# Kernel optimization log

Measured on AMD Instinct MI355X. Metric: run time of the kernel, lower is better.

The kernel has to match this reference:

```python
import jax, jax.numpy as jnp
import numpy as np

B = 32768
D_IN = 512      # input_dim == dict_dim (forced by the STE add)
HID = 512       # hard-coded hidden width of linear1
D = 512         # dict_dim / embedding_dim
P = 8           # per_factor_dict_size: number of codebooks / MLP branches
K = 10          # num_factor: codebook size (rows per embedding table)
COMMIT = 0.25


def setup_inputs() -> dict:
    key = jax.random.key(0)
    ks = jax.random.split(key, 7)
    s1 = 1.0 / np.sqrt(D_IN)
    s2 = 1.0 / np.sqrt(HID)
    return {
        "inputs": jax.random.normal(ks[0], (B, D_IN), jnp.float32),
        "W1": jax.random.uniform(ks[1], (P, HID, D_IN), jnp.float32, -s1, s1),
        "b1": jax.random.uniform(ks[2], (P, HID), jnp.float32, -s1, s1),
        "W2": jax.random.uniform(ks[3], (P, D, HID), jnp.float32, -s2, s2),
        "b2": jax.random.uniform(ks[4], (P, D), jnp.float32, -s2, s2),
        # embedding init: uniform(-1/num_factor, 1/num_factor)
        "E": jax.random.uniform(ks[5], (P, K, D), jnp.float32, -1.0 / K, 1.0 / K),
        "label_gen": jax.random.randint(ks[6], (B,), 0, K, jnp.int64),
    }


def reference(inputs, W1, b1, W2, b2, E, label_gen):
    sg = jax.lax.stop_gradient
    # P parallel 2-layer MLPs: [P, B, D]
    h = jax.nn.relu(jnp.einsum("bd,phd->pbh", inputs, W1) + b1[:, None, :])
    z = jnp.einsum("pbh,peh->pbe", h, W2) + b2[:, None, :]
    # squared-distance expansion per codebook: [P, B, K]
    distances = (
        jnp.sum(z * z, axis=-1, keepdims=True)
        + jnp.sum(E * E, axis=-1)[:, None, :]
        - 2.0 * jnp.einsum("pbd,pkd->pbk", z, E)
    )
    ave_distances = jnp.mean(distances, axis=0)          # [B, K]
    idx = jnp.argmin(ave_distances, axis=1)              # [B]
    # one-hot @ E[p] then mean over p == mean codebook gathered at idx
    Emean = jnp.mean(E, axis=0)                          # [K, D]
    vq = Emean[idx]                                      # [B, D]
    vq_z = inputs + sg(vq - inputs)                      # straight-through
    # all_vq_z[j] = mean_p E[p, j]; losses vs every code row: [K, B]
    diff1 = Emean[:, None, :] - sg(inputs)[None, :, :]   # [K, B, D]
    diff2 = sg(Emean)[:, None, :] - inputs[None, :, :]
    all_vq_loss = jnp.sum(diff1 * diff1, axis=-1) + COMMIT * jnp.sum(diff2 * diff2, axis=-1)
    all_vq_z = inputs[None, :, :] + sg(Emean[:, None, :] - inputs[None, :, :])  # [K, B, D]
    changed_vq_z = Emean[label_gen]                      # [B, D]
    return (vq_z, distances, all_vq_z, all_vq_loss, changed_vq_z)
```

## Files before the change

kernel.cpp:

```cpp
#include <hip/hip_runtime.h>
#include <stdint.h>

typedef _Float16 f16;
typedef _Float16 f16x4 __attribute__((ext_vector_type(4)));
typedef _Float16 f16x8 __attribute__((ext_vector_type(8)));
typedef float f32x4 __attribute__((ext_vector_type(4)));

#define B_ROWS 32768
#define DIM 512
#define NP 8
#define NK 10

typedef __attribute__((address_space(3))) unsigned int lds_u32;
typedef __attribute__((address_space(1))) const unsigned int gbl_u32;

__device__ __forceinline__ void gload_lds16(const void* g, void* l) {
  __builtin_amdgcn_global_load_lds((gbl_u32*)(uintptr_t)g, (lds_u32*)(uintptr_t)l, 16, 0, 0);
}


__global__ void prep_split(const float4* __restrict__ X4, f16x4* __restrict__ Xh4,
                           f16x4* __restrict__ Xl4, const float4* __restrict__ W14,
                           f16x4* __restrict__ W1h4, f16x4* __restrict__ W1l4,
                           const float4* __restrict__ W24, f16x4* __restrict__ W2h4) {
  int bid = blockIdx.x, tid = threadIdx.x;
  if (bid < 1024) {
    for (int i = bid * 256 + tid; i < 4194304; i += 1024 * 256) {
      float4 v = X4[i];
      f16x4 h = {(f16)v.x, (f16)v.y, (f16)v.z, (f16)v.w};
      f16x4 l = {(f16)(v.x - (float)h[0]), (f16)(v.y - (float)h[1]),
                 (f16)(v.z - (float)h[2]), (f16)(v.w - (float)h[3])};
      Xh4[i] = h;
      Xl4[i] = l;
    }
  } else if (bid < 1152) {
    for (int i = (bid - 1024) * 256 + tid; i < 524288; i += 128 * 256) {
      float4 v = W14[i];
      f16x4 h = {(f16)v.x, (f16)v.y, (f16)v.z, (f16)v.w};
      f16x4 l = {(f16)(v.x - (float)h[0]), (f16)(v.y - (float)h[1]),
                 (f16)(v.z - (float)h[2]), (f16)(v.w - (float)h[3])};
      W1h4[i] = h;
      W1l4[i] = l;
    }
  } else {
    for (int i = (bid - 1152) * 256 + tid; i < 524288; i += 128 * 256) {
      float4 v = W24[i];
      f16x4 h = {(f16)v.x, (f16)v.y, (f16)v.z, (f16)v.w};
      W2h4[i] = h;
    }
  }
}


__global__ void enorm2(const float* __restrict__ E, float* __restrict__ Emean,
                       float* __restrict__ E2, float* __restrict__ E2m) {
  int bid = blockIdx.x;
  int lane = threadIdx.x;
  if (bid < 80) {
    const float* src = E + (size_t)bid * DIM;
    float s = 0.f;
    for (int i = lane; i < DIM; i += 64) {
      float v = src[i];
      s = fmaf(v, v, s);
    }
#pragma unroll
    for (int m = 1; m < 64; m <<= 1) s += __shfl_xor(s, m, 64);
    if (lane == 0) E2[bid] = s;
  } else {
    int k = bid - 80;
    float acc = 0.f;
    for (int i = lane; i < DIM; i += 64) {
      float s = 0.f;
#pragma unroll
      for (int p = 0; p < NP; ++p) s += E[p * NK * DIM + k * DIM + i];
      s *= 0.125f;
      Emean[k * DIM + i] = s;
      acc = fmaf(s, s, acc);
    }
#pragma unroll
    for (int m = 1; m < 64; m <<= 1) acc += __shfl_xor(acc, m, 64);
    if (lane == 0) E2m[k] = acc;
  }
}


__global__ __launch_bounds__(512) void etilde_kernel(const float* __restrict__ W2,
                                                     const float* __restrict__ b2,
                                                     const float* __restrict__ E,
                                                     f16* __restrict__ EimgH,
                                                     f16* __restrict__ EimgL,
                                                     float* __restrict__ c_) {
  const int p = blockIdx.x / NK, k = blockIdx.x % NK;
  const int h = threadIdx.x;
  __shared__ float Er[512];
  __shared__ float red[8];
  Er[h] = E[((size_t)p * NK + k) * DIM + h];
  __syncthreads();
  const float* Wp = W2 + (size_t)p * DIM * DIM;
  float s = 0.f;
#pragma unroll 8
  for (int d = 0; d < DIM; ++d) s = fmaf(Wp[(size_t)d * DIM + h], Er[d], s);
  int ei = p * 8320 + k * 520 + h;
  f16 hi = (f16)s;
  EimgH[ei] = hi;
  EimgL[ei] = (f16)(s - (float)hi);
  if (h < 8) {
    int pi = p * 8320 + k * 520 + 512 + h;
    EimgH[pi] = (f16)0.f;
    EimgL[pi] = (f16)0.f;
  }
  if (k == 0) {
    for (int j = h; j < 6 * 520; j += 512) {
      int pi = p * 8320 + 10 * 520 + j;
      EimgH[pi] = (f16)0.f;
      EimgL[pi] = (f16)0.f;
    }
  }
  float t = b2[p * DIM + h] * Er[h];
#pragma unroll
  for (int m = 1; m < 64; m <<= 1) t += __shfl_xor(t, m, 64);
  if ((h & 63) == 0) red[h >> 6] = t;
  __syncthreads();
  if (h == 0) {
    float cc = 0.f;
#pragma unroll
    for (int i = 0; i < 8; ++i) cc += red[i];
    c_[p * NK + k] = cc;
  }
}


template <int EPI, int NBN, int NPROD, int GRP>
__global__ __launch_bounds__(256) void gemmA(
    const f16* __restrict__ Ah_, const f16* __restrict__ Al_, int lda, int apitch,
    const f16* __restrict__ Bh_, const f16* __restrict__ Bl_, int bpitch,
    const float* __restrict__ bias_, int bias_pitch,
    f16* __restrict__ Oh, f16* __restrict__ Ol, int ldo,
    float* __restrict__ part2) {
  __shared__ f16 smem[32768];
  const int tid = threadIdx.x;
  const int lane = tid & 63;
  const int wave = tid >> 6;
  const int wr = wave >> 1, wc = wave & 1;
  const int p = blockIdx.z;

  const int q8 = gridDim.x >> 3;
  const int bid = blockIdx.x;
  const int swz = (bid & 7) * q8 + (bid >> 3);
  const int band = swz / (GRP * NBN);
  const int r_ = swz % (GRP * NBN);
  const int bm = band * GRP + (r_ % GRP);
  const int bn = r_ / GRP;
  const int m0 = bm * 128, n0 = bn * 128;

  const f16* Ahp = Ah_ + (size_t)p * apitch;
  const f16* Alp = Al_ + (size_t)p * apitch;
  const f16* Bhp = Bh_ + (size_t)p * bpitch;
  const f16* Blp = Bl_ + (size_t)p * bpitch;

  const int NT = (NPROD == 3) ? 24 : 8;

  f32x4 acc[4][4] = {};

  auto stage = [&](int buf, int t) {
    const f16* As;
    const f16* Bs;
    int k0;
    if (NPROD == 3) {
      int pr = t % 3;
      As = (pr == 2) ? Alp : Ahp;
      Bs = (pr == 1) ? Blp : Bhp;
      k0 = (t / 3) * 64;
    } else {
      As = Ahp;
      Bs = Bhp;
      k0 = t * 64;
    }
    f16* sA = smem + buf * 16384;
    f16* sB = sA + 8192;
#pragma unroll
    for (int j = 0; j < 4; ++j) {
      int r = j * 32 + (tid >> 3);
      int c = ((tid & 7) ^ (r & 7)) * 8;
      gload_lds16(As + (size_t)(m0 + r) * lda + k0 + c, sA + j * 2048 + tid * 8);
      gload_lds16(Bs + (size_t)(n0 + r) * 512 + k0 + c, sB + j * 2048 + tid * 8);
    }
  };

  stage(0, 0);
  __syncthreads();

  const int g = lane >> 4, rl = lane & 15;

  for (int s = 0; s < NT; ++s) {
    int nx = s + 1;
    if (nx < NT) stage(nx & 1, nx);
    const char* sA = (const char*)(smem + (s & 1) * 16384);
    const char* sB = sA + 16384;
    f16x8 af[4][2], bf[4][2];
#pragma unroll
    for (int i = 0; i < 4; ++i) {
      int ra = wr * 64 + i * 16 + rl;
      int rb = wc * 64 + i * 16 + rl;
#pragma unroll
      for (int kk = 0; kk < 2; ++kk) {
        int cb = kk * 64 + g * 16;
        af[i][kk] = *(const f16x8*)(sA + ra * 128 + (cb ^ ((ra & 7) << 4)));
        bf[i][kk] = *(const f16x8*)(sB + rb * 128 + (cb ^ ((rb & 7) << 4)));
      }
    }
#pragma unroll
    for (int i = 0; i < 4; ++i)
#pragma unroll
      for (int jn = 0; jn < 4; ++jn)
#pragma unroll
        for (int kk = 0; kk < 2; ++kk)
          acc[i][jn] = __builtin_amdgcn_mfma_f32_16x16x32_f16(af[i][kk], bf[jn][kk], acc[i][jn], 0, 0, 0);
    __syncthreads();
  }

  if (EPI == 0) {
#pragma unroll
    for (int jn = 0; jn < 4; ++jn) {
      int cg = n0 + wc * 64 + jn * 16 + rl;
      float bv = bias_[cg];
#pragma unroll
      for (int i = 0; i < 4; ++i) {
        int r0 = m0 + wr * 64 + i * 16 + g * 4;
#pragma unroll
        for (int r = 0; r < 4; ++r) {
          float z = acc[i][jn][r] + bv;
          z = fmaxf(z, 0.f);
          f16 h = (f16)z;
          size_t off = (size_t)(r0 + r) * ldo + cg;
          Oh[off] = h;
          Ol[off] = (f16)(z - (float)h);
        }
      }
    }
  } else {
    const float* bp = bias_ + (size_t)p * bias_pitch;
    float bvals[4];
#pragma unroll
    for (int jn = 0; jn < 4; ++jn) bvals[jn] = bp[n0 + wc * 64 + jn * 16 + rl];
    const int ch = bn * 2 + wc;
    float* pb = part2 + (size_t)(p * 8 + ch) * B_ROWS;
#pragma unroll
    for (int i = 0; i < 4; ++i) {
#pragma unroll
      for (int r = 0; r < 4; ++r) {
        float q = 0.f;
#pragma unroll
        for (int jn = 0; jn < 4; ++jn) {
          float z = acc[i][jn][r] + bvals[jn];
          q = fmaf(z, z, q);
        }
#pragma unroll
        for (int m = 1; m < 16; m <<= 1) q += __shfl_xor(q, m, 64);
        if (rl == 0) pb[m0 + wr * 64 + i * 16 + g * 4 + r] = q;
      }
    }
  }
}


__global__ __launch_bounds__(256) void g2d_union(
    const f16* __restrict__ Hh, const f16* __restrict__ Hl,
    const f16* __restrict__ W2h, const float* __restrict__ b2,
    const f16* __restrict__ EimgH, const f16* __restrict__ EimgL,
    const float* __restrict__ c_, float* __restrict__ part2,
    float* __restrict__ gout) {
  __shared__ char pool[66048];
  const int tid = threadIdx.x;
  const int p = blockIdx.y;

  if (blockIdx.x < 1024) {
    f16* smem = (f16*)pool;
    const int lane = tid & 63, wave = tid >> 6;
    const int wr = wave >> 1, wc = wave & 1;
    const int bid = blockIdx.x;
    const int swz = (bid & 7) * 128 + (bid >> 3);
    const int bm = swz >> 2, bn = swz & 3;
    const int m0 = bm * 128, n0 = bn * 128;
    const f16* Ahp = Hh + (size_t)p * 512;
    const f16* Bhp = W2h + (size_t)p * 262144;

    f32x4 acc[4][4] = {};

    auto stage = [&](int buf, int t) {
      int k0 = t * 64;
      f16* sA = smem + buf * 16384;
      f16* sB = sA + 8192;
#pragma unroll
      for (int j = 0; j < 4; ++j) {
        int r = j * 32 + (tid >> 3);
        int c = ((tid & 7) ^ (r & 7)) * 8;
        gload_lds16(Ahp + (size_t)(m0 + r) * 4096 + k0 + c, sA + j * 2048 + tid * 8);
        gload_lds16(Bhp + (size_t)(n0 + r) * 512 + k0 + c, sB + j * 2048 + tid * 8);
      }
    };

    stage(0, 0);
    __syncthreads();
    const int g = lane >> 4, rl = lane & 15;
    for (int s = 0; s < 8; ++s) {
      if (s + 1 < 8) stage((s + 1) & 1, s + 1);
      const char* sA = (const char*)(smem + (s & 1) * 16384);
      const char* sB = sA + 16384;
      f16x8 af[4][2], bf[4][2];
#pragma unroll
      for (int i = 0; i < 4; ++i) {
        int ra = wr * 64 + i * 16 + rl;
        int rb = wc * 64 + i * 16 + rl;
#pragma unroll
        for (int kk = 0; kk < 2; ++kk) {
          int cb = kk * 64 + g * 16;
          af[i][kk] = *(const f16x8*)(sA + ra * 128 + (cb ^ ((ra & 7) << 4)));
          bf[i][kk] = *(const f16x8*)(sB + rb * 128 + (cb ^ ((rb & 7) << 4)));
        }
      }
#pragma unroll
      for (int i = 0; i < 4; ++i)
#pragma unroll
        for (int jn = 0; jn < 4; ++jn)
#pragma unroll
          for (int kk = 0; kk < 2; ++kk)
            acc[i][jn] = __builtin_amdgcn_mfma_f32_16x16x32_f16(af[i][kk], bf[jn][kk], acc[i][jn], 0, 0, 0);
      __syncthreads();
    }

    const float* bp = b2 + (size_t)p * 512;
    float bvals[4];
#pragma unroll
    for (int jn = 0; jn < 4; ++jn) bvals[jn] = bp[n0 + wc * 64 + jn * 16 + rl];
    const int ch = bn * 2 + wc;
    float* pb = part2 + (size_t)(p * 8 + ch) * B_ROWS;
#pragma unroll
    for (int i = 0; i < 4; ++i) {
#pragma unroll
      for (int r = 0; r < 4; ++r) {
        float q = 0.f;
#pragma unroll
        for (int jn = 0; jn < 4; ++jn) {
          float z = acc[i][jn][r] + bvals[jn];
          q = fmaf(z, z, q);
        }
#pragma unroll
        for (int m = 1; m < 16; m <<= 1) q += __shfl_xor(q, m, 64);
        if (rl == 0) pb[m0 + wr * 64 + i * 16 + g * 4 + r] = q;
      }
    }
  } else {
    f16* sH = (f16*)pool;
    f16* sL = (f16*)(pool + 16384);
    f16* sEh = (f16*)(pool + 32768);
    f16* sEl = (f16*)(pool + 49408);
    const int lane = tid & 63, wave = tid >> 6;
    const int r0 = (blockIdx.x - 1024) * 64;
    {
      const uint32_t* ih = (const uint32_t*)(EimgH + (size_t)p * 16 * 520);
      const uint32_t* il = (const uint32_t*)(EimgL + (size_t)p * 16 * 520);
      uint32_t* oh = (uint32_t*)sEh;
      uint32_t* ol = (uint32_t*)sEl;
      for (int i = tid; i < 16 * 520 / 2; i += 256) {
        oh[i] = ih[i];
        ol[i] = il[i];
      }
    }
    const int gq = lane >> 4, rl = lane & 15;

    auto stageT = [&](int buf, int t) {
#pragma unroll
      for (int rnd = 0; rnd < 2; ++rnd) {
        int w = rnd * 256 + tid;
        int r = w >> 3;
        int c = ((w & 7) ^ (r & 7)) * 8;
        gload_lds16(Hh + (size_t)(r0 + r) * 4096 + p * DIM + t * 64 + c,
                    sH + buf * 4096 + (size_t)w * 8);
        gload_lds16(Hl + (size_t)(r0 + r) * 4096 + p * DIM + t * 64 + c,
                    sL + buf * 4096 + (size_t)w * 8);
      }
    };

    f32x4 acc = {};
    stageT(0, 0);
    __syncthreads();

    for (int t = 0; t < 8; ++t) {
      if (t < 7) stageT((t + 1) & 1, t + 1);
      const char* bh = (const char*)(sH + (t & 1) * 4096);
      const char* bl = (const char*)(sL + (t & 1) * 4096);
      const int ra = wave * 16 + rl;
      f16x8 ah[2], al[2], beh[2], bel[2];
#pragma unroll
      for (int kk = 0; kk < 2; ++kk) {
        int cb = kk * 64 + gq * 16;
        ah[kk] = *(const f16x8*)(bh + ra * 128 + (cb ^ ((ra & 7) << 4)));
        al[kk] = *(const f16x8*)(bl + ra * 128 + (cb ^ ((ra & 7) << 4)));
        int ce = t * 128 + kk * 64 + gq * 16;
        beh[kk] = *(const f16x8*)((const char*)sEh + rl * 1040 + ce);
        bel[kk] = *(const f16x8*)((const char*)sEl + rl * 1040 + ce);
      }
#pragma unroll
      for (int kk = 0; kk < 2; ++kk) {
        acc = __builtin_amdgcn_mfma_f32_16x16x32_f16(ah[kk], beh[kk], acc, 0, 0, 0);
        acc = __builtin_amdgcn_mfma_f32_16x16x32_f16(ah[kk], bel[kk], acc, 0, 0, 0);
        acc = __builtin_amdgcn_mfma_f32_16x16x32_f16(al[kk], beh[kk], acc, 0, 0, 0);
      }
      __syncthreads();
    }
    if (rl < NK) {
      float cv = c_[p * NK + rl];
#pragma unroll
      for (int r = 0; r < 4; ++r) {
        int row = r0 + wave * 16 + gq * 4 + r;
        gout[((size_t)p * B_ROWS + row) * NK + rl] = acc[r] + cv;
      }
    }
  }
}


__global__ __launch_bounds__(256) void final_kernel(
    const float* __restrict__ X, const float* __restrict__ part2,
    float* __restrict__ gdist, const float* __restrict__ E2,
    const float* __restrict__ Emean, const float* __restrict__ E2m,
    const int* __restrict__ label, float* __restrict__ vq_z,
    float* __restrict__ avz, float* __restrict__ loss, float* __restrict__ changed) {
  __shared__ float Em[NK * DIM];
  __shared__ float e2s[NK];
  const int tid = threadIdx.x;
  for (int i = tid; i < NK * DIM; i += 256) Em[i] = Emean[i];
  if (tid < NK) e2s[tid] = E2m[tid];
  __syncthreads();

  const int b0 = blockIdx.x * 16;
  {
    const float4* Em4 = (const float4*)Em;
    float4* avz4 = (float4*)avz;
    if (blockIdx.x < 256) {
      for (int it = 0; it < 80; ++it) {
        int idx = it * 256 + tid;
        int d4 = idx & 127, row = (idx >> 7) & 15, k = idx >> 11;
        if (k == 8) continue;
        avz4[(((size_t)k * B_ROWS + b0 + row) << 7) + d4] = Em4[k * 128 + d4];
      }
    } else {
      for (int it = 0; it < 80; ++it) {
        int idx = it * 256 + tid;
        int d4 = idx & 127, row = (idx >> 7) & 15, k = idx >> 11;
        avz4[(((size_t)k * B_ROWS + b0 + row) << 7) + d4] = Em4[k * 128 + d4];
      }
    }
  }

  const int lane = tid & 63, wave = tid >> 6;
  const int pl = lane & 7, kh = lane >> 3;
  for (int rr = 0; rr < 4; ++rr) {
    int b = b0 + wave * 4 + rr;
    float zq = part2[(size_t)(pl * 8 + kh) * B_ROWS + b];
    zq += __shfl_xor(zq, 8, 64);
    zq += __shfl_xor(zq, 16, 64);
    zq += __shfl_xor(zq, 32, 64);
    float g0 = gdist[((size_t)pl * B_ROWS + b) * NK + kh];
    float g1 = (lane < 16) ? gdist[((size_t)pl * B_ROWS + b) * NK + 8 + kh] : 0.f;
    float dv0 = zq + E2[pl * NK + kh] - 2.f * g0;
    float dv1 = zq + E2[pl * NK + 8 + kh] - 2.f * g1;
    gdist[((size_t)pl * B_ROWS + b) * NK + kh] = dv0;
    if (lane < 16) gdist[((size_t)pl * B_ROWS + b) * NK + 8 + kh] = dv1;
    float v0 = dv0, v1 = (lane < 16) ? dv1 : 0.f;
#pragma unroll
    for (int m = 1; m < 8; m <<= 1) {
      v0 += __shfl_xor(v0, m, 64);
      v1 += __shfl_xor(v1, m, 64);
    }
    float a[NK];
#pragma unroll
    for (int k = 0; k < 8; ++k) a[k] = __shfl(v0, k * 8, 64);
    a[8] = __shfl(v1, 0, 64);
    a[9] = __shfl(v1, 8, 64);
    int idx = 0;
    float mn = a[0];
#pragma unroll
    for (int k = 1; k < NK; ++k) {
      if (a[k] < mn) { mn = a[k]; idx = k; }
    }
    const float* xr = X + (size_t)b * DIM;
    float sx = 0.f, dx[NK] = {};
#pragma unroll
    for (int j = 0; j < 8; ++j) {
      float x = xr[j * 64 + lane];
      sx = fmaf(x, x, sx);
#pragma unroll
      for (int k = 0; k < NK; ++k) dx[k] = fmaf(x, Em[k * DIM + j * 64 + lane], dx[k]);
    }
#pragma unroll
    for (int m = 1; m < 64; m <<= 1) {
      sx += __shfl_xor(sx, m, 64);
#pragma unroll
      for (int k = 0; k < NK; ++k) dx[k] += __shfl_xor(dx[k], m, 64);
    }
    if (lane == 0) {
#pragma unroll
      for (int k = 0; k < NK; ++k)
        loss[(size_t)k * B_ROWS + b] = 1.25f * (sx - 2.f * dx[k] + e2s[k]);
    }
    int lab = label[b];
#pragma unroll
    for (int j = 0; j < 8; ++j) {
      int c = j * 64 + lane;
      vq_z[(size_t)b * DIM + c] = Em[idx * DIM + c];
      changed[(size_t)b * DIM + c] = Em[lab * DIM + c];
    }
  }
}


__global__ void bcast_rest(const float* __restrict__ Emean, float4* __restrict__ avz4) {
  const float4* Em4 = (const float4*)Emean;
  int tid = blockIdx.x * 256 + threadIdx.x;
  for (int it = 0; it < 32; ++it) {
    int idx = tid + it * 16384;
    int b = idx >> 7, d4 = idx & 127;
    avz4[((size_t)(8 * B_ROWS + b) << 7) + d4] = Em4[8 * 128 + d4];
  }
}


extern "C" void kernel_launch(void* const* d_in, const int* in_sizes, int n_in,
                              void* d_out, int out_size, void* d_ws, size_t ws_size,
                              hipStream_t stream) {
  const float* X = (const float*)d_in[0];
  const float* W1 = (const float*)d_in[1];
  const float* b1 = (const float*)d_in[2];
  const float* W2 = (const float*)d_in[3];
  const float* b2 = (const float*)d_in[4];
  const float* E = (const float*)d_in[5];
  const int* lab = (const int*)d_in[6];
  float* out = (float*)d_out;

  float* vq_z = out;
  float* dist = out + 16777216;
  float* avz = out + 16777216 + 2621440;
  float* loss = avz + 167772160;
  float* chg = loss + 327680;

  f16* Xh = (f16*)vq_z;
  f16* Xl = Xh + 16777216;
  f16* Hh = (f16*)avz;
  f16* Hl = Hh + 134217728;
  float* part2 = avz + 134217728;

  char* w = (char*)d_ws;
  f16* W1h = (f16*)w; w += 4194304;
  f16* W1l = (f16*)w; w += 4194304;
  f16* W2h = (f16*)w; w += 4194304;
  float* Emean = (float*)w; w += NK * DIM * 4;
  float* E2 = (float*)w; w += 512;
  float* E2m = (float*)w; w += 256;
  float* c_ = (float*)w; w += 512;
  f16* EimgH = (f16*)w; w += NP * 16 * 520 * 2;
  f16* EimgL = (f16*)w; w += NP * 16 * 520 * 2;

  prep_split<<<1280, 256, 0, stream>>>((const float4*)X, (f16x4*)Xh, (f16x4*)Xl,
                                       (const float4*)W1, (f16x4*)W1h, (f16x4*)W1l,
                                       (const float4*)W2, (f16x4*)W2h);
  enorm2<<<90, 64, 0, stream>>>(E, Emean, E2, E2m);
  etilde_kernel<<<80, 512, 0, stream>>>(W2, b2, E, EimgH, EimgL, c_);

  gemmA<0, 32, 3, 8><<<dim3(8192, 1, 1), 256, 0, stream>>>(
      Xh, Xl, 512, 0, W1h, W1l, 0, b1, 0, Hh, Hl, 4096, nullptr);

  g2d_union<<<dim3(1536, NP), 256, 0, stream>>>(Hh, Hl, W2h, b2, EimgH, EimgL, c_,
                                                part2, dist);

  final_kernel<<<2048, 256, 0, stream>>>(X, part2, dist, E2, Emean, E2m, lab,
                                         vq_z, avz, loss, chg);
  bcast_rest<<<64, 256, 0, stream>>>(Emean, (float4*)avz);
}
```

Baseline: 1.065 ms.

## Restructure first GEMM to stage hi/lo splits together and reuse fragments

The first-layer GEMM used to stream three separate passes (hi*hi, hi*lo, lo*hi) as 24 K-steps of 64, reloading A and B fragments for each product. It now loads Ah, Al, Bh and Bl for a 32-wide K slice into one LDS stage and issues all three MFMA products from the same register fragments over 16 steps. This cuts global/LDS traffic and barriers per useful MFMA, and uses a new swizzle for the 64-byte rows. The unused EPI=1 epilogue and the per-p template generality are removed.

```diff
diff --git a/kernel.cpp b/kernel.cpp
--- a/kernel.cpp
+++ b/kernel.cpp
@@ -130,19 +130,17 @@
 }
 
 
-template <int EPI, int NBN, int NPROD, int GRP>
-__global__ __launch_bounds__(256) void gemmA(
-    const f16* __restrict__ Ah_, const f16* __restrict__ Al_, int lda, int apitch,
-    const f16* __restrict__ Bh_, const f16* __restrict__ Bl_, int bpitch,
-    const float* __restrict__ bias_, int bias_pitch,
-    f16* __restrict__ Oh, f16* __restrict__ Ol, int ldo,
-    float* __restrict__ part2) {
+template <int NBN, int GRP>
+__global__ __launch_bounds__(256) void gemm1_k32(
+    const f16* __restrict__ Ah_, const f16* __restrict__ Al_,
+    const f16* __restrict__ Bh_, const f16* __restrict__ Bl_,
+    const float* __restrict__ bias_,
+    f16* __restrict__ Oh, f16* __restrict__ Ol, int ldo) {
   __shared__ f16 smem[32768];
   const int tid = threadIdx.x;
   const int lane = tid & 63;
   const int wave = tid >> 6;
   const int wr = wave >> 1, wc = wave & 1;
-  const int p = blockIdx.z;
 
   const int q8 = gridDim.x >> 3;
   const int bid = blockIdx.x;
@@ -153,37 +151,20 @@
   const int bn = r_ / GRP;
   const int m0 = bm * 128, n0 = bn * 128;
 
-  const f16* Ahp = Ah_ + (size_t)p * apitch;
-  const f16* Alp = Al_ + (size_t)p * apitch;
-  const f16* Bhp = Bh_ + (size_t)p * bpitch;
-  const f16* Blp = Bl_ + (size_t)p * bpitch;
-
-  const int NT = (NPROD == 3) ? 24 : 8;
-
   f32x4 acc[4][4] = {};
 
-  auto stage = [&](int buf, int t) {
-    const f16* As;
-    const f16* Bs;
-    int k0;
-    if (NPROD == 3) {
-      int pr = t % 3;
-      As = (pr == 2) ? Alp : Ahp;
-      Bs = (pr == 1) ? Blp : Bhp;
-      k0 = (t / 3) * 64;
-    } else {
-      As = Ahp;
-      Bs = Bhp;
-      k0 = t * 64;
-    }
-    f16* sA = smem + buf * 16384;
-    f16* sB = sA + 8192;
-#pragma unroll
-    for (int j = 0; j < 4; ++j) {
-      int r = j * 32 + (tid >> 3);
-      int c = ((tid & 7) ^ (r & 7)) * 8;
-      gload_lds16(As + (size_t)(m0 + r) * lda + k0 + c, sA + j * 2048 + tid * 8);
-      gload_lds16(Bs + (size_t)(n0 + r) * 512 + k0 + c, sB + j * 2048 + tid * 8);
+  auto stage = [&](int buf, int s) {
+    int k0 = s * 32;
+    f16* base = smem + buf * 16384;
+#pragma unroll
+    for (int rnd = 0; rnd < 2; ++rnd) {
+      int w = rnd * 256 + tid;
+      int r = w >> 2;
+      int c = ((w & 3) ^ ((r >> 1) & 3)) * 8;
+      gload_lds16(Ah_ + (size_t)(m0 + r) * 512 + k0 + c, base + (size_t)w * 8);
+      gload_lds16(Al_ + (size_t)(m0 + r) * 512 + k0 + c, base + 4096 + (size_t)w * 8);
+      gload_lds16(Bh_ + (size_t)(n0 + r) * 512 + k0 + c, base + 8192 + (size_t)w * 8);
+      gload_lds16(Bl_ + (size_t)(n0 + r) * 512 + k0 + c, base + 12288 + (size_t)w * 8);
     }
   };
 
@@ -192,72 +173,47 @@
 
   const int g = lane >> 4, rl = lane & 15;
 
-  for (int s = 0; s < NT; ++s) {
-    int nx = s + 1;
-    if (nx < NT) stage(nx & 1, nx);
-    const char* sA = (const char*)(smem + (s & 1) * 16384);
-    const char* sB = sA + 16384;
+  for (int s = 0; s < 16; ++s) {
+    if (s + 1 < 16) stage((s + 1) & 1, s + 1);
+    const char* base = (const char*)(smem + (s & 1) * 16384);
     f16x8 af[4][2], bf[4][2];
 #pragma unroll
     for (int i = 0; i < 4; ++i) {
       int ra = wr * 64 + i * 16 + rl;
+      int offa = ra * 64 + ((g ^ ((ra >> 1) & 3)) << 4);
+      af[i][0] = *(const f16x8*)(base + offa);
+      af[i][1] = *(const f16x8*)(base + 8192 + offa);
       int rb = wc * 64 + i * 16 + rl;
-#pragma unroll
-      for (int kk = 0; kk < 2; ++kk) {
-        int cb = kk * 64 + g * 16;
-        af[i][kk] = *(const f16x8*)(sA + ra * 128 + (cb ^ ((ra & 7) << 4)));
-        bf[i][kk] = *(const f16x8*)(sB + rb * 128 + (cb ^ ((rb & 7) << 4)));
-      }
+      int offb = rb * 64 + ((g ^ ((rb >> 1) & 3)) << 4);
+      bf[i][0] = *(const f16x8*)(base + 16384 + offb);
+      bf[i][1] = *(const f16x8*)(base + 24576 + offb);
     }
 #pragma unroll
     for (int i = 0; i < 4; ++i)
 #pragma unroll
-      for (int jn = 0; jn < 4; ++jn)
-#pragma unroll
-        for (int kk = 0; kk < 2; ++kk)
-          acc[i][jn] = __builtin_amdgcn_mfma_f32_16x16x32_f16(af[i][kk], bf[jn][kk], acc[i][jn], 0, 0, 0);
+      for (int jn = 0; jn < 4; ++jn) {
+        acc[i][jn] = __builtin_amdgcn_mfma_f32_16x16x32_f16(af[i][0], bf[jn][0], acc[i][jn], 0, 0, 0);
+        acc[i][jn] = __builtin_amdgcn_mfma_f32_16x16x32_f16(af[i][0], bf[jn][1], acc[i][jn], 0, 0, 0);
+        acc[i][jn] = __builtin_amdgcn_mfma_f32_16x16x32_f16(af[i][1], bf[jn][0], acc[i][jn], 0, 0, 0);
+      }
     __syncthreads();
   }
 
-  if (EPI == 0) {
-#pragma unroll
-    for (int jn = 0; jn < 4; ++jn) {
-      int cg = n0 + wc * 64 + jn * 16 + rl;
-      float bv = bias_[cg];
-#pragma unroll
-      for (int i = 0; i < 4; ++i) {
-        int r0 = m0 + wr * 64 + i * 16 + g * 4;
-#pragma unroll
-        for (int r = 0; r < 4; ++r) {
-          float z = acc[i][jn][r] + bv;
-          z = fmaxf(z, 0.f);
-          f16 h = (f16)z;
-          size_t off = (size_t)(r0 + r) * ldo + cg;
-          Oh[off] = h;
-          Ol[off] = (f16)(z - (float)h);
-        }
-      }
-    }
-  } else {
-    const float* bp = bias_ + (size_t)p * bias_pitch;
-    float bvals[4];
-#pragma unroll
-    for (int jn = 0; jn < 4; ++jn) bvals[jn] = bp[n0 + wc * 64 + jn * 16 + rl];
-    const int ch = bn * 2 + wc;
-    float* pb = part2 + (size_t)(p * 8 + ch) * B_ROWS;
+#pragma unroll
+  for (int jn = 0; jn < 4; ++jn) {
+    int cg = n0 + wc * 64 + jn * 16 + rl;
+    float bv = bias_[cg];
 #pragma unroll
     for (int i = 0; i < 4; ++i) {
+      int r0 = m0 + wr * 64 + i * 16 + g * 4;
 #pragma unroll
       for (int r = 0; r < 4; ++r) {
-        float q = 0.f;
-#pragma unroll
-        for (int jn = 0; jn < 4; ++jn) {
-          float z = acc[i][jn][r] + bvals[jn];
-          q = fmaf(z, z, q);
-        }
-#pragma unroll
-        for (int m = 1; m < 16; m <<= 1) q += __shfl_xor(q, m, 64);
-        if (rl == 0) pb[m0 + wr * 64 + i * 16 + g * 4 + r] = q;
+        float z = acc[i][jn][r] + bv;
+        z = fmaxf(z, 0.f);
+        f16 h = (f16)z;
+        size_t off = (size_t)(r0 + r) * ldo + cg;
+        Oh[off] = h;
+        Ol[off] = (f16)(z - (float)h);
       }
     }
   }
@@ -568,8 +524,8 @@
   enorm2<<<90, 64, 0, stream>>>(E, Emean, E2, E2m);
   etilde_kernel<<<80, 512, 0, stream>>>(W2, b2, E, EimgH, EimgL, c_);
 
-  gemmA<0, 32, 3, 8><<<dim3(8192, 1, 1), 256, 0, stream>>>(
-      Xh, Xl, 512, 0, W1h, W1l, 0, b1, 0, Hh, Hl, 4096, nullptr);
+  gemm1_k32<32, 8><<<dim3(8192, 1, 1), 256, 0, stream>>>(
+      Xh, Xl, W1h, W1l, b1, Hh, Hl, 4096);
 
   g2d_union<<<dim3(1536, NP), 256, 0, stream>>>(Hh, Hl, W2h, b2, EimgH, EimgL, c_,
                                                 part2, dist);
```

Result: no change. 1.085 ms (median of 2 runs) (+1.8%).
